# Kernel optimization log

Hardware: AMD Instinct MI355X
Metric: run time of the kernel (lower is better)

## Reference

```python
import jax, jax.numpy as jnp
import numpy as np
import math

# hyperparams matching init_kwargs
GAMMA_S = 0.8
GAMMA_U = 0.8
RHO_I = 0.1
RHO_T = 0.1
EPS = 1e-10
TAU_MIN = 0.005
TAU_MAX = 1.0
TAU_INIT = 0.07
GRAD_CLIP = 5.0
ETA_INIT = 0.01
ETA_MIN = 0.0001
N_STATE = 2900000
BSZ = 4096
DIM = 1024


def setup_inputs() -> dict:
    key = jax.random.key(0)
    k1, k2 = jax.random.split(key)
    imf = jax.random.normal(k1, (BSZ, DIM), jnp.float32)
    imf = imf / jnp.linalg.norm(imf, axis=1, keepdims=True)
    txf = jax.random.normal(k2, (BSZ, DIM), jnp.float32)
    txf = txf / jnp.linalg.norm(txf, axis=1, keepdims=True)
    return {
        "image_features": imf,
        "text_features": txf,
        "s_I": jnp.zeros((N_STATE,), jnp.float32),
        "s_T": jnp.zeros((N_STATE,), jnp.float32),
        "tau_I": jnp.full((N_STATE,), TAU_INIT, jnp.float32),
        "tau_T": jnp.full((N_STATE,), TAU_INIT, jnp.float32),
        "u_I": jnp.zeros((N_STATE,), jnp.float32),
        "u_T": jnp.zeros((N_STATE,), jnp.float32),
        "b_I": jnp.zeros((N_STATE,), jnp.float32),
        "b_T": jnp.zeros((N_STATE,), jnp.float32),
        "image_ids": jnp.arange(BSZ, dtype=jnp.int32),
        "text_ids": jnp.arange(BSZ, dtype=jnp.int32),
        "epoch": 5,
        "max_epoch": 30,
    }


def reference(image_features, text_features, s_I, s_T, tau_I, tau_T,
              u_I, u_T, b_I, b_T, image_ids, text_ids, epoch, max_epoch):
    B = image_features.shape[0]
    sim = jnp.einsum('id,jd->ij', image_features, text_features)  # [B,B]
    diag_sim = jnp.diagonal(sim)                                  # [B]

    tau_image = tau_I[image_ids]  # [B]
    tau_text = tau_T[text_ids]    # [B]

    image_diffs = sim - diag_sim[:, None]
    text_diffs = sim - diag_sim[None, :]
    # .detach() in torch -> stop_gradient
    idt = jax.lax.stop_gradient(image_diffs / tau_image[:, None])
    tdt = jax.lax.stop_gradient(text_diffs / tau_text[None, :])

    # max-trick state b_I / b_T: running row/col max per sample id
    old_b_I = b_I[image_ids]
    new_b_I = jnp.maximum(jnp.max(idt, axis=1), old_b_I)  # [B]
    old_b_T = b_T[text_ids]
    new_b_T = jnp.maximum(jnp.max(tdt, axis=0), old_b_T)  # [B]

    exp_image_diffs = jnp.exp(idt - new_b_I[:, None])
    exp_text_diffs = jnp.exp(tdt - new_b_T[None, :])
    g_I = jnp.sum(exp_image_diffs, axis=1, keepdims=True) / (B - 1)  # [B,1]
    g_T = jnp.sum(exp_text_diffs, axis=0, keepdims=True) / (B - 1)   # [1,B]

    # moving-average s state (compute_last=False, last_g_* = None path)
    s_I_new = (1.0 - GAMMA_S) * s_I[image_ids] * jnp.exp(old_b_I - new_b_I) + GAMMA_S * g_I[:, 0]
    s_T_new = (1.0 - GAMMA_S) * s_T[text_ids] * jnp.exp(old_b_T - new_b_T) + GAMMA_S * g_T[0, :]
    s_I_b = s_I_new[:, None]  # same shape as g_I
    s_T_b = s_T_new[None, :]  # same shape as g_T

    weights_image = exp_image_diffs / (s_I_b + EPS)
    weights_text = exp_text_diffs / (s_T_b + EPS)

    image_loss = jnp.sum(weights_image * image_diffs, axis=1, keepdims=True) / (B - 1)
    text_loss = jnp.sum(weights_text * text_diffs, axis=0, keepdims=True) / (B - 1)
    total_loss = image_loss.mean() + text_loss.mean()

    grad_tau_image = (jnp.log(s_I_b) + new_b_I[:, None] + RHO_I
                      - jnp.sum(weights_image * idt, axis=1, keepdims=True) / (B - 1))
    grad_tau_text = (jnp.log(s_T_b) + new_b_T[None, :] + RHO_T
                     - jnp.sum(weights_text * tdt, axis=0, keepdims=True) / (B - 1))

    u_I_new = (1.0 - GAMMA_U) * u_I[image_ids] + GAMMA_U * jnp.clip(grad_tau_image[:, 0], -GRAD_CLIP, GRAD_CLIP)
    u_T_new = (1.0 - GAMMA_U) * u_T[text_ids] + GAMMA_U * jnp.clip(grad_tau_text[0, :], -GRAD_CLIP, GRAD_CLIP)

    eta_cur = ETA_MIN + (ETA_INIT - ETA_MIN) * math.cos(math.pi * (epoch / max_epoch) / 2)
    tau_I_new = jnp.clip(tau_image - eta_cur * u_I_new, TAU_MIN, TAU_MAX)
    tau_T_new = jnp.clip(tau_text - eta_cur * u_T_new, TAU_MIN, TAU_MAX)

    # scattered state writes (the module's in-place buffer updates)
    b_I_out = b_I.at[image_ids].set(new_b_I)
    b_T_out = b_T.at[text_ids].set(new_b_T)
    s_I_out = s_I.at[image_ids].set(s_I_new)
    s_T_out = s_T.at[text_ids].set(s_T_new)
    u_I_out = u_I.at[image_ids].set(u_I_new)
    u_T_out = u_T.at[text_ids].set(u_T_new)
    tau_I_out = tau_I.at[image_ids].set(tau_I_new)
    tau_T_out = tau_T.at[text_ids].set(tau_T_new)

    avg_image_tau = tau_image.mean()
    avg_text_tau = tau_text.mean()

    return (g_I, g_T, grad_tau_image, grad_tau_text, total_loss,
            avg_image_tau, avg_text_tau,
            s_I_out, s_T_out, u_I_out, u_T_out,
            b_I_out, b_T_out, tau_I_out, tau_T_out)
```

## Files before the change

kernel.cpp:

```cpp
#include <hip/hip_runtime.h>
#include <math.h>

#define BSZ 4096
#define DIM 1024
#define NST 2900000

constexpr float GAMMA_S   = 0.8f;
constexpr float GAMMA_U   = 0.8f;
constexpr float RHO_I_C   = 0.1f;
constexpr float RHO_T_C   = 0.1f;
constexpr float C_EPS     = 1e-10f;
constexpr float TAU_MIN_C = 0.005f;
constexpr float TAU_MAX_C = 1.0f;
constexpr float GCLIP     = 5.0f;
constexpr float ETA_INIT_C = 0.01f;
constexpr float ETA_MIN_C  = 1e-4f;
constexpr float PI_F       = 3.14159265358979323846f;

typedef __bf16 bf16x8 __attribute__((ext_vector_type(8)));
typedef float  f32x4  __attribute__((ext_vector_type(4)));

__device__ __forceinline__ unsigned short f2bf(float f) {
    unsigned int u = __float_as_uint(f);
    u += 0x7fffu + ((u >> 16) & 1u);
    return (unsigned short)(u >> 16);
}
__device__ __forceinline__ float bf2f(unsigned short s) {
    return __uint_as_float(((unsigned int)s) << 16);
}

__global__ __launch_bounds__(256) void conv_diag(const float* __restrict__ imf,
                                                 const float* __restrict__ txf,
                                                 unsigned short* __restrict__ abf,
                                                 unsigned short* __restrict__ bbf,
                                                 const float* __restrict__ tau_I,
                                                 const float* __restrict__ tau_T,
                                                 const float* __restrict__ b_I,
                                                 const float* __restrict__ b_T,
                                                 const int* __restrict__ iid,
                                                 const int* __restrict__ tid_,
                                                 float* diag, float* tauIg, float* tauTg,
                                                 float* obI, float* obT,
                                                 float* __restrict__ scal) {
    if (blockIdx.x == 0 && threadIdx.x < 3) scal[threadIdx.x] = 0.f;
    const int w  = threadIdx.x >> 6;
    const int ln = threadIdx.x & 63;
    const int i  = blockIdx.x * 4 + w;
    float dot = 0.f;
#pragma unroll
    for (int k = 0; k < 4; ++k) {
        const int off = i * DIM + k * 256 + ln * 4;
        const f32x4 a = __builtin_nontemporal_load((const f32x4*)&imf[off]);
        const f32x4 b = __builtin_nontemporal_load((const f32x4*)&txf[off]);
        ushort4 ra, rb;
        ra.x = f2bf(a.x); ra.y = f2bf(a.y); ra.z = f2bf(a.z); ra.w = f2bf(a.w);
        rb.x = f2bf(b.x); rb.y = f2bf(b.y); rb.z = f2bf(b.z); rb.w = f2bf(b.w);
        *(ushort4*)&abf[off] = ra;
        *(ushort4*)&bbf[off] = rb;
        dot += bf2f(ra.x) * bf2f(rb.x) + bf2f(ra.y) * bf2f(rb.y) +
               bf2f(ra.z) * bf2f(rb.z) + bf2f(ra.w) * bf2f(rb.w);
    }
#pragma unroll
    for (int m = 32; m; m >>= 1) dot += __shfl_xor(dot, m);
    if (ln == 0) {
        diag[i] = dot;
        const int id = iid[i];
        tauIg[i] = tau_I[id];
        obI[i]   = b_I[id];
        const int td = tid_[i];
        tauTg[i] = tau_T[td];
        obT[i]   = b_T[td];
    }
}

__device__ __forceinline__ void async16(const void* g, void* l) {
    __builtin_amdgcn_global_load_lds(
        (const __attribute__((address_space(1))) void*)g,
        (__attribute__((address_space(3))) void*)l, 16, 0, 0);
}

__global__ __launch_bounds__(256) void gemm_fused(const unsigned short* __restrict__ A,
                                                  const unsigned short* __restrict__ B,
                                                  const float* __restrict__ diag,
                                                  const float* __restrict__ tauIg,
                                                  const float* __restrict__ tauTg,
                                                  float* __restrict__ rpM,
                                                  float* __restrict__ rpE,
                                                  float* __restrict__ rpV,
                                                  float* __restrict__ cpM,
                                                  float* __restrict__ cpE,
                                                  float* __restrict__ cpV,
                                                  const float* __restrict__ s_I,
                                                  const float* __restrict__ s_T,
                                                  const float* __restrict__ u_I,
                                                  const float* __restrict__ u_T,
                                                  const float* __restrict__ b_I,
                                                  const float* __restrict__ b_T,
                                                  const float* __restrict__ tau_I,
                                                  const float* __restrict__ tau_T,
                                                  float* __restrict__ outbase) {
    __shared__ unsigned short As[128 * 32];
    __shared__ unsigned short Bs[128 * 32];

    const int tid = threadIdx.x;
    const int gid = ((blockIdx.x >> 4) << 3) | (blockIdx.x & 7);

    if ((blockIdx.x >> 3) & 1) {
        const size_t idx = (size_t)gid * 256 + tid;
        const size_t stride = (size_t)1024 * 256;
        const size_t NV = (NST - 1) / 4;
        const float* srcs[8] = {s_I, s_T, u_I, u_T, b_I, b_T, tau_I, tau_T};
#pragma unroll
        for (int a = 0; a < 8; ++a) {
            const float* s = srcs[a];
            float* d = outbase + (size_t)a * NST;
            size_t c = idx;
            for (; c + stride < NV; c += 2 * stride) {
                const size_t c2 = c + stride;
                const f32x4 f0 = __builtin_nontemporal_load((const f32x4*)&s[4 * c]);
                const f32x4 f1 = __builtin_nontemporal_load((const f32x4*)&s[4 * c2]);
                const float nx0 = __builtin_nontemporal_load(&s[4 * c + 4]);
                const float nx1 = __builtin_nontemporal_load(&s[4 * c2 + 4]);
                f32x4 v0; v0.x = f0.y; v0.y = f0.z; v0.z = f0.w; v0.w = nx0;
                f32x4 v1; v1.x = f1.y; v1.y = f1.z; v1.z = f1.w; v1.w = nx1;
                __builtin_nontemporal_store(v0, (f32x4*)&d[1 + 4 * c]);
                __builtin_nontemporal_store(v1, (f32x4*)&d[1 + 4 * c2]);
            }
            if (c < NV) {
                const f32x4 f = __builtin_nontemporal_load((const f32x4*)&s[4 * c]);
                const float nx = __builtin_nontemporal_load(&s[4 * c + 4]);
                f32x4 v; v.x = f.y; v.y = f.z; v.z = f.w; v.w = nx;
                __builtin_nontemporal_store(v, (f32x4*)&d[1 + 4 * c]);
            }
            if (idx == 0) d[0] = s[0];
            if (idx < 3)  d[NST - 3 + idx] = s[NST - 3 + idx];
        }
        return;
    }

    const int bjIdx = gid & 31, biIdx = gid >> 5;
    const int bi = biIdx * 128;
    const int bj = bjIdx * 128;
    const int lane = tid & 63;
    const int wave = tid >> 6;
    const int m_base = (wave >> 1) * 64;
    const int n_base = (wave & 1) * 64;

    const int c0 = tid, c1 = tid + 256;
    const int r0 = c0 >> 2, kg0 = ((c0 & 3) ^ ((r0 >> 1) & 3)) * 8;
    const int r1 = c1 >> 2, kg1 = ((c1 & 3) ^ ((r1 >> 1) & 3)) * 8;

    f32x4 acc[4][4];
#pragma unroll
    for (int m = 0; m < 4; ++m)
#pragma unroll
        for (int n = 0; n < 4; ++n)
            acc[m][n] = (f32x4){0.f, 0.f, 0.f, 0.f};

    const int mrow = lane & 15;
    const int q    = lane >> 4;

    for (int k0 = 0; k0 < DIM; k0 += 32) {
        __syncthreads();
        async16(&A[(size_t)(bi + r0) * DIM + k0 + kg0], &As[c0 * 8]);
        async16(&A[(size_t)(bi + r1) * DIM + k0 + kg1], &As[c1 * 8]);
        async16(&B[(size_t)(bj + r0) * DIM + k0 + kg0], &Bs[c0 * 8]);
        async16(&B[(size_t)(bj + r1) * DIM + k0 + kg1], &Bs[c1 * 8]);
        __syncthreads();

        __builtin_amdgcn_s_setprio(1);
        bf16x8 af[4], bfr[4];
#pragma unroll
        for (int t = 0; t < 4; ++t) {
            const int rlA = m_base + t * 16 + mrow;
            const int rlB = n_base + t * 16 + mrow;
            af[t]  = *(const bf16x8*)&As[rlA * 32 + (q ^ ((rlA >> 1) & 3)) * 8];
            bfr[t] = *(const bf16x8*)&Bs[rlB * 32 + (q ^ ((rlB >> 1) & 3)) * 8];
        }
#pragma unroll
        for (int mt = 0; mt < 4; ++mt)
#pragma unroll
            for (int nt = 0; nt < 4; ++nt)
                acc[mt][nt] = __builtin_amdgcn_mfma_f32_16x16x32_bf16(
                    af[mt], bfr[nt], acc[mt][nt], 0, 0, 0);
        __builtin_amdgcn_s_setprio(0);
    }

    __syncthreads();
    float* prm = (float*)Bs;
    if (tid < 128) {
        prm[tid]       = diag[bi + tid];
        prm[128 + tid] = 1.0f / tauIg[bi + tid];
        prm[256 + tid] = diag[bj + tid];
        prm[384 + tid] = 1.0f / tauTg[bj + tid];
    }
    __syncthreads();

    float* red = (float*)As;
    const int rowq = (lane >> 4) * 4;

#pragma unroll
    for (int mt = 0; mt < 4; ++mt)
#pragma unroll
        for (int r = 0; r < 4; ++r) {
            const int row_l = m_base + mt * 16 + rowq + r;
            const float dgr = prm[row_l];
            const float itr = prm[128 + row_l];
            float v0 = (acc[mt][0][r] - dgr) * itr;
            float v1 = (acc[mt][1][r] - dgr) * itr;
            float v2 = (acc[mt][2][r] - dgr) * itr;
            float v3 = (acc[mt][3][r] - dgr) * itr;
            float m = fmaxf(fmaxf(v0, v1), fmaxf(v2, v3));
#pragma unroll
            for (int x = 1; x <= 8; x <<= 1) m = fmaxf(m, __shfl_xor(m, x));
            const float e0 = __expf(v0 - m), e1 = __expf(v1 - m);
            const float e2 = __expf(v2 - m), e3 = __expf(v3 - m);
            float se = e0 + e1 + e2 + e3;
            float sv = e0 * v0 + e1 * v1 + e2 * v2 + e3 * v3;
#pragma unroll
            for (int x = 1; x <= 8; x <<= 1) {
                se += __shfl_xor(se, x);
                sv += __shfl_xor(sv, x);
            }
            if ((lane & 15) == 0) {
                const int idx = wave * 64 + mt * 16 + rowq + r;
                red[idx] = m; red[256 + idx] = se; red[512 + idx] = sv;
            }
        }

#pragma unroll
    for (int nt = 0; nt < 4; ++nt) {
        const int col_l = n_base + nt * 16 + (lane & 15);
        const float dgc = prm[256 + col_l];
        const float itc = prm[384 + col_l];
        float m = -INFINITY;
#pragma unroll
        for (int mt = 0; mt < 4; ++mt)
#pragma unroll
            for (int r = 0; r < 4; ++r)
                m = fmaxf(m, (acc[mt][nt][r] - dgc) * itc);
        m = fmaxf(m, __shfl_xor(m, 16));
        m = fmaxf(m, __shfl_xor(m, 32));
        float se = 0.f, sv = 0.f;
#pragma unroll
        for (int mt = 0; mt < 4; ++mt)
#pragma unroll
            for (int r = 0; r < 4; ++r) {
                const float v = (acc[mt][nt][r] - dgc) * itc;
                const float e = __expf(v - m);
                se += e; sv += e * v;
            }
        se += __shfl_xor(se, 16); se += __shfl_xor(se, 32);
        sv += __shfl_xor(sv, 16); sv += __shfl_xor(sv, 32);
        if (lane < 16) {
            const int idx = wave * 64 + nt * 16 + lane;
            red[768 + idx] = m; red[1024 + idx] = se; red[1280 + idx] = sv;
        }
    }
    __syncthreads();

    if (tid < 128) {
        const int rg = tid, li = rg & 63;
        const int w0 = (rg >> 6) * 2, w1 = w0 + 1;
        const float mA = red[w0 * 64 + li], mB = red[w1 * 64 + li];
        const float M = fmaxf(mA, mB);
        const float fA = __expf(mA - M), fB = __expf(mB - M);
        const size_t o = (size_t)bjIdx * BSZ + bi + rg;
        rpM[o] = M;
        rpE[o] = red[256 + w0 * 64 + li] * fA + red[256 + w1 * 64 + li] * fB;
        rpV[o] = red[512 + w0 * 64 + li] * fA + red[512 + w1 * 64 + li] * fB;
    } else {
        const int cg = tid - 128, li = cg & 63;
        const int w0 = cg >> 6, w1 = w0 + 2;
        const float mA = red[768 + w0 * 64 + li], mB = red[768 + w1 * 64 + li];
        const float M = fmaxf(mA, mB);
        const float fA = __expf(mA - M), fB = __expf(mB - M);
        const size_t o = (size_t)biIdx * BSZ + bj + cg;
        cpM[o] = M;
        cpE[o] = red[1024 + w0 * 64 + li] * fA + red[1024 + w1 * 64 + li] * fB;
        cpV[o] = red[1280 + w0 * 64 + li] * fA + red[1280 + w1 * 64 + li] * fB;
    }
}

__global__ __launch_bounds__(256) void finalize(const float* __restrict__ s_I,
                                                const float* __restrict__ s_T,
                                                const float* __restrict__ u_I,
                                                const float* __restrict__ u_T,
                                                const int* __restrict__ iid,
                                                const int* __restrict__ tid_,
                                                const int* __restrict__ epoch,
                                                const int* __restrict__ maxep,
                                                const float* __restrict__ tauIg,
                                                const float* __restrict__ tauTg,
                                                const float* __restrict__ obI,
                                                const float* __restrict__ obT,
                                                const float* __restrict__ rpM,
                                                const float* __restrict__ rpE,
                                                const float* __restrict__ rpV,
                                                const float* __restrict__ cpM,
                                                const float* __restrict__ cpE,
                                                const float* __restrict__ cpV,
                                                float* __restrict__ out) {
    const int side = blockIdx.x & 1;
    const int i0   = (blockIdx.x >> 1) * 64;
    const int w    = threadIdx.x >> 6;
    const int il   = threadIdx.x & 63;
    const int i    = i0 + il;

    const float* pM  = side ? cpM  : rpM;
    const float* pE  = side ? cpE  : rpE;
    const float* pV  = side ? cpV  : rpV;
    const float* tg  = side ? tauTg : tauIg;
    const float* obA = side ? obT  : obI;
    const float* sA  = side ? s_T  : s_I;
    const float* uA  = side ? u_T  : u_I;
    const int*   ids = side ? tid_ : iid;
    const float  rho = side ? RHO_T_C : RHO_I_C;

    float M[8], E[8], V[8];
#pragma unroll
    for (int k = 0; k < 8; ++k) {
        const size_t o = (size_t)(w * 8 + k) * BSZ + i;
        M[k] = pM[o]; E[k] = pE[o]; V[k] = pV[o];
    }
    float pm = M[0];
#pragma unroll
    for (int k = 1; k < 8; ++k) pm = fmaxf(pm, M[k]);

    __shared__ float lred[12][64];
    lred[w][il] = pm;
    __syncthreads();

    const float ob = obA[i];
    const float nb = fmaxf(fmaxf(fmaxf(lred[0][il], lred[1][il]),
                                 fmaxf(lred[2][il], lred[3][il])), ob);
    float se = 0.f, sv = 0.f;
#pragma unroll
    for (int k = 0; k < 8; ++k) {
        const float f = __expf(M[k] - nb);
        se += E[k] * f;
        sv += V[k] * f;
    }
    lred[4 + w][il] = se;
    lred[8 + w][il] = sv;
    __syncthreads();

    if (w == 0) {
        const float eta = ETA_MIN_C + (ETA_INIT_C - ETA_MIN_C) *
                          cosf(0.5f * PI_F * ((float)epoch[0] / (float)maxep[0]));
        const float invBm1 = 1.0f / (float)(BSZ - 1);
        const float invB   = 1.0f / (float)BSZ;

        const int   id  = ids[i];
        const float tau = tg[i];
        const float seT = (lred[4][il] + lred[5][il]) + (lred[6][il] + lred[7][il]);
        const float svT = (lred[8][il] + lred[9][il]) + (lred[10][il] + lred[11][il]);

        const float g     = seT * invBm1;
        const float s_new = (1.f - GAMMA_S) * sA[id] * __expf(ob - nb) + GAMMA_S * g;
        const float W     = svT * invBm1 / (s_new + C_EPS);
        const float grad  = logf(s_new) + nb + rho - W;
        const float gc    = fminf(fmaxf(grad, -GCLIP), GCLIP);
        const float u_new = (1.f - GAMMA_U) * uA[id] + GAMMA_U * gc;
        const float tau_new = fminf(fmaxf(tau - eta * u_new, TAU_MIN_C), TAU_MAX_C);

        float* stb   = out + 4 * BSZ + 3;
        float* o_g   = out + side * BSZ;
        float* o_gt  = out + (2 + side) * BSZ;
        float* o_s   = stb + (size_t)side * NST;
        float* o_u   = stb + (size_t)(2 + side) * NST;
        float* o_b   = stb + (size_t)(4 + side) * NST;
        float* o_t   = stb + (size_t)(6 + side) * NST;

        o_g[i]  = g;
        o_gt[i] = grad;
        o_s[id] = s_new;
        o_u[id] = u_new;
        o_b[id] = nb;
        o_t[id] = tau_new;

        float v0 = tau * W * invB;
        float v1 = tau * invB;
#pragma unroll
        for (int o2 = 32; o2; o2 >>= 1) {
            v0 += __shfl_down(v0, o2);
            v1 += __shfl_down(v1, o2);
        }
        if (il == 0) {
            atomicAdd(&out[4 * BSZ + 0], v0);
            atomicAdd(&out[4 * BSZ + 1 + side], v1);
        }
    }
}

extern "C" void kernel_launch(void* const* d_in, const int* in_sizes, int n_in,
                              void* d_out, int out_size, void* d_ws, size_t ws_size,
                              hipStream_t stream) {
    const float* imf   = (const float*)d_in[0];
    const float* txf   = (const float*)d_in[1];
    const float* s_I   = (const float*)d_in[2];
    const float* s_T   = (const float*)d_in[3];
    const float* tau_I = (const float*)d_in[4];
    const float* tau_T = (const float*)d_in[5];
    const float* u_I   = (const float*)d_in[6];
    const float* u_T   = (const float*)d_in[7];
    const float* b_I   = (const float*)d_in[8];
    const float* b_T   = (const float*)d_in[9];
    const int* iid     = (const int*)d_in[10];
    const int* tid_    = (const int*)d_in[11];
    const int* epoch   = (const int*)d_in[12];
    const int* maxep   = (const int*)d_in[13];

    float* out = (float*)d_out;
    float* ws  = (float*)d_ws;

    float* diag  = ws + 0 * BSZ;
    float* tauIg = ws + 1 * BSZ;
    float* tauTg = ws + 2 * BSZ;
    float* obI   = ws + 3 * BSZ;
    float* obT   = ws + 4 * BSZ;
    float* rpM   = ws + 5 * BSZ;
    float* rpE   = rpM + (size_t)32 * BSZ;
    float* rpV   = rpE + (size_t)32 * BSZ;
    float* cpM   = rpV + (size_t)32 * BSZ;
    float* cpE   = cpM + (size_t)32 * BSZ;
    float* cpV   = cpE + (size_t)32 * BSZ;
    unsigned short* abf = (unsigned short*)(cpV + (size_t)32 * BSZ);
    unsigned short* bbf = abf + (size_t)BSZ * DIM;

    conv_diag<<<BSZ / 4, 256, 0, stream>>>(imf, txf, abf, bbf, tau_I, tau_T, b_I, b_T,
                                           iid, tid_, diag, tauIg, tauTg, obI, obT,
                                           out + 4 * BSZ);
    gemm_fused<<<2048, 256, 0, stream>>>(abf, bbf, diag, tauIg, tauTg,
                                         rpM, rpE, rpV, cpM, cpE, cpV,
                                         s_I, s_T, u_I, u_T, b_I, b_T, tau_I, tau_T,
                                         out + 4 * BSZ + 3);
    finalize<<<128, 256, 0, stream>>>(s_I, s_T, u_I, u_T, iid, tid_, epoch, maxep,
                                      tauIg, tauTg, obI, obT,
                                      rpM, rpE, rpV, cpM, cpE, cpV, out);
}
```

Measured before the change: 274.1 us.

## Double-buffer LDS tiles to overlap global loads with MFMA compute

```diff
diff --git a/kernel.cpp b/kernel.cpp
--- a/kernel.cpp
+++ b/kernel.cpp
@@ -99,8 +99,8 @@
                                                   const float* __restrict__ tau_I,
                                                   const float* __restrict__ tau_T,
                                                   float* __restrict__ outbase) {
-    __shared__ unsigned short As[128 * 32];
-    __shared__ unsigned short Bs[128 * 32];
+    __shared__ unsigned short As[2][128 * 32];
+    __shared__ unsigned short Bs[2][128 * 32];
 
     const int tid = threadIdx.x;
     const int gid = ((blockIdx.x >> 4) << 3) | (blockIdx.x & 7);
@@ -160,22 +160,33 @@
     const int mrow = lane & 15;
     const int q    = lane >> 4;
 
-    for (int k0 = 0; k0 < DIM; k0 += 32) {
-        __syncthreads();
-        async16(&A[(size_t)(bi + r0) * DIM + k0 + kg0], &As[c0 * 8]);
-        async16(&A[(size_t)(bi + r1) * DIM + k0 + kg1], &As[c1 * 8]);
-        async16(&B[(size_t)(bj + r0) * DIM + k0 + kg0], &Bs[c0 * 8]);
-        async16(&B[(size_t)(bj + r1) * DIM + k0 + kg1], &Bs[c1 * 8]);
-        __syncthreads();
+#define STG(bsel, kk0)                                                             \
+    {                                                                              \
+        async16(&A[(size_t)(bi + r0) * DIM + (kk0) + kg0], &As[bsel][c0 * 8]);     \
+        async16(&A[(size_t)(bi + r1) * DIM + (kk0) + kg1], &As[bsel][c1 * 8]);     \
+        async16(&B[(size_t)(bj + r0) * DIM + (kk0) + kg0], &Bs[bsel][c0 * 8]);     \
+        async16(&B[(size_t)(bj + r1) * DIM + (kk0) + kg1], &Bs[bsel][c1 * 8]);     \
+    }
+
+    STG(0, 0);
+    for (int t = 0; t < 32; ++t) {
+        const int cur = t & 1;
+        if (t < 31) {
+            STG(cur ^ 1, (t + 1) * 32);
+            asm volatile("s_waitcnt vmcnt(4)" ::: "memory");
+        } else {
+            asm volatile("s_waitcnt vmcnt(0)" ::: "memory");
+        }
+        __builtin_amdgcn_s_barrier();
 
         __builtin_amdgcn_s_setprio(1);
         bf16x8 af[4], bfr[4];
 #pragma unroll
-        for (int t = 0; t < 4; ++t) {
-            const int rlA = m_base + t * 16 + mrow;
-            const int rlB = n_base + t * 16 + mrow;
-            af[t]  = *(const bf16x8*)&As[rlA * 32 + (q ^ ((rlA >> 1) & 3)) * 8];
-            bfr[t] = *(const bf16x8*)&Bs[rlB * 32 + (q ^ ((rlB >> 1) & 3)) * 8];
+        for (int tt = 0; tt < 4; ++tt) {
+            const int rlA = m_base + tt * 16 + mrow;
+            const int rlB = n_base + tt * 16 + mrow;
+            af[tt]  = *(const bf16x8*)&As[cur][rlA * 32 + (q ^ ((rlA >> 1) & 3)) * 8];
+            bfr[tt] = *(const bf16x8*)&Bs[cur][rlB * 32 + (q ^ ((rlB >> 1) & 3)) * 8];
         }
 #pragma unroll
         for (int mt = 0; mt < 4; ++mt)
@@ -184,7 +195,11 @@
                 acc[mt][nt] = __builtin_amdgcn_mfma_f32_16x16x32_bf16(
                     af[mt], bfr[nt], acc[mt][nt], 0, 0, 0);
         __builtin_amdgcn_s_setprio(0);
-    }
+
+        asm volatile("s_waitcnt lgkmcnt(0)" ::: "memory");
+        __builtin_amdgcn_s_barrier();
+    }
+#undef STG
 
     __syncthreads();
     float* prm = (float*)Bs;
```

Measured after the change: 300.6 us. 9.7% more time.
